# Optimization experiments

Hardware: AMD Instinct MI355X
Metric: run time of the kernel (lower is better)

Reference implementation:

```python
import jax, jax.numpy as jnp
import numpy as np

N = 100000   # nodes per layer
E = 600000   # edges per block
FIN = 256    # raw feature dim
H = 128      # hidden_size
C = 47       # n_classes
L = 3        # num_layers = n_layers + 1
NOUT = 10000 # seed nodes
GEN_EPS = 1e-7
T = 1.0
LN_EPS = 1e-5


def setup_inputs() -> dict:
    key = jax.random.key(0)
    ks = jax.random.split(key, 10)
    return {
        "x": jax.random.normal(ks[0], (N, FIN), jnp.float32),
        "src": jax.random.randint(ks[1], (L - 1, E), 0, N),
        "dst": jax.random.randint(ks[2], (L - 1, E), 0, N),
        "node_map": jax.random.randint(ks[3], (L - 1, N), 0, N),
        "final_map": jax.random.randint(ks[4], (NOUT,), 0, N),
        "enc_w": jax.random.normal(ks[5], (FIN, H), jnp.float32) * 0.05,
        "enc_b": jnp.zeros((H,), jnp.float32),
        "gcn_w": jax.random.normal(ks[6], (L, H, H), jnp.float32) * 0.05,
        "gcn_b": jnp.zeros((L, H), jnp.float32),
        "ln_g": jnp.ones((L, H), jnp.float32),
        "ln_b": jnp.zeros((L, H), jnp.float32),
        "pred_w": jax.random.normal(ks[7], (H, C), jnp.float32) * 0.05,
        "pred_b": jnp.zeros((C,), jnp.float32),
    }


def _layer_norm(h, g, b):
    mu = jnp.mean(h, axis=-1, keepdims=True)
    var = jnp.mean(jnp.square(h - mu), axis=-1, keepdims=True)
    return (h - mu) * jax.lax.rsqrt(var + LN_EPS) * g + b


def _gen_conv(h, src, dst, w, b):
    # GENConv, aggr='softmax', mlp_layers=1, no edge_attr, no msg_norm.
    m = jax.nn.relu(h[src]) + GEN_EPS                      # [E, H] messages
    # per-destination, per-feature segment softmax with temperature T
    mx = jax.ops.segment_max(m * T, dst, num_segments=N)   # [N, H]
    e = jnp.exp(m * T - mx[dst])                           # [E, H]
    denom = jax.ops.segment_sum(e, dst, num_segments=N)    # [N, H]
    alpha = e / (denom[dst] + 1e-16)
    agg = jax.ops.segment_sum(m * alpha, dst, num_segments=N)  # [N, H]
    return (agg + h) @ w + b                               # residual + Linear (MLP)


def reference(x, src, dst, node_map, final_map, enc_w, enc_b,
              gcn_w, gcn_b, ln_g, ln_b, pred_w, pred_b):
    h = x @ enc_w + enc_b                                  # node_features_encoder
    h = _gen_conv(h, src[0], dst[0], gcn_w[0], gcn_b[0])   # gcns[0] with block-0 edges
    for layer in range(1, L):                              # res+ block
        h2 = jax.nn.relu(_layer_norm(h, ln_g[layer - 1], ln_b[layer - 1]))
        # dropout is identity in eval mode (p applied with training=False)
        # gcns[layer] uses the edge_index set BEFORE this iteration's move
        h = _gen_conv(h2, src[layer - 1], dst[layer - 1],
                      gcn_w[layer], gcn_b[layer]) + h
        h = h[node_map[layer - 1]]                         # nf_move_layer_to gather
    h = jax.nn.relu(_layer_norm(h, ln_g[L - 1], ln_b[L - 1]))
    h = h @ pred_w + pred_b                                # node_pred_linear
    h = h[final_map]                                       # seed-node extraction
    return jax.nn.log_softmax(h, axis=-1)
```

## Files before the change

kernel.cpp:

```cpp
#include <hip/hip_runtime.h>
#include <hip/hip_bf16.h>
#include <hip/hip_fp16.h>

typedef unsigned short u16;
typedef unsigned int u32;

#define N_NODES 100000
#define N_EDGES 600000
#define FIN_D   256
#define HDIM    128
#define NCLS    47
#define NOUT_D  10000
#define NCHUNK  196
#define NP2     100352
#define PCH     2048
#define PNB     ((N_EDGES + PCH - 1) / PCH)
#define EB      1024

typedef short bf16x8 __attribute__((ext_vector_type(8)));
typedef float f32x4  __attribute__((ext_vector_type(4)));

#define GPTR(p) (const __attribute__((address_space(1))) u32*)(p)
#define LPTR(p) (__attribute__((address_space(3))) u32*)(p)

__device__ __forceinline__ float bf2f(u16 u) {
    union { u32 i; float f; } v; v.i = ((u32)u) << 16; return v.f;
}
__device__ __forceinline__ u16 f2bf(float f) {
    __hip_bfloat16 h = __float2bfloat16(f);
    return *reinterpret_cast<u16*>(&h);
}
__device__ __forceinline__ float loadF(const void* p, size_t i, bool f32) {
    if (f32) return ((const float*)p)[i];
    return bf2f(((const u16*)p)[i]);
}
__device__ __forceinline__ float wave_sum(float v) {
    #pragma unroll
    for (int o = 32; o > 0; o >>= 1) v += __shfl_xor(v, o, 64);
    return v;
}
__device__ __forceinline__ float wave_max(float v) {
    #pragma unroll
    for (int o = 32; o > 0; o >>= 1) v = fmaxf(v, __shfl_xor(v, o, 64));
    return v;
}
__device__ __forceinline__ int block_excl_scan_256(int v, int* wsum) {
    int lane = threadIdx.x & 63, wv = threadIdx.x >> 6;
    int inc = v;
    #pragma unroll
    for (int off = 1; off < 64; off <<= 1) {
        int u = __shfl_up(inc, off, 64);
        if (lane >= off) inc += u;
    }
    if (lane == 63) wsum[wv] = inc;
    __syncthreads();
    if (threadIdx.x == 0) {
        int a = 0;
        #pragma unroll
        for (int w = 0; w < 4; ++w) { int t = wsum[w]; wsum[w] = a; a += t; }
    }
    __syncthreads();
    return inc - v + wsum[wv];
}

__global__ __launch_bounds__(256) void dtype_detect_kernel(
    const u16* __restrict__ x, int* __restrict__ flag)
{
    int i = blockIdx.x * 256 + threadIdx.x;
    u32 e = (x[i] >> 7) & 0xFF;
    unsigned long long b = __ballot(e >= 200);
    if ((threadIdx.x & 63) == 0) {
        int c = __popcll(b);
        if (c) atomicAdd(&flag[1], c);
    }
}

__global__ __launch_bounds__(256) void histb_kernel(
    const int* __restrict__ dst, int* __restrict__ bcnt, int ebgrid)
{
    __shared__ int h[NCHUNK];
    int half = (blockIdx.x >= ebgrid) ? 1 : 0;
    int e0 = (blockIdx.x - half * ebgrid) * EB;
    for (int i = threadIdx.x; i < NCHUNK; i += 256) h[i] = 0;
    __syncthreads();
    #pragma unroll
    for (int t = 0; t < 4; ++t) {
        int e = e0 + t * 256 + threadIdx.x;
        if (e < N_EDGES) atomicAdd(&h[dst[half * N_EDGES + e] >> 9], 1);
    }
    __syncthreads();
    for (int i = threadIdx.x; i < NCHUNK; i += 256)
        if (h[i]) atomicAdd(&bcnt[half * NCHUNK + i], h[i]);
}

__global__ __launch_bounds__(256) void coff2_kernel(
    const int* __restrict__ csum, int* __restrict__ coff,
    int* __restrict__ bcur)
{
    __shared__ int wsum[4];
    int t = threadIdx.x;
    for (int h = 0; h < 2; ++h) {
        int v = (t < NCHUNK) ? csum[h * NCHUNK + t] : 0;
        int excl = block_excl_scan_256(v, wsum);
        if (t < NCHUNK) {
            coff[h * NCHUNK + t] = excl;
            bcur[(h * NCHUNK + t) * 16] = excl;
        }
        __syncthreads();
    }
}

__global__ __launch_bounds__(256) void bucket_part_kernel(
    const int* __restrict__ src, const int* __restrict__ dst,
    const int* __restrict__ comp1,
    int* __restrict__ bcur, int2* __restrict__ tmp)
{
    __shared__ int hist[NCHUNK];
    __shared__ int base[NCHUNK];
    int half = (blockIdx.x >= PNB) ? 1 : 0;
    int b = blockIdx.x - half * PNB;
    int e0 = b * PCH;
    for (int i = threadIdx.x; i < NCHUNK; i += 256) hist[i] = 0;
    __syncthreads();

    int2 loc[8];
    #pragma unroll
    for (int t = 0; t < 8; ++t) {
        int e = e0 + t * 256 + threadIdx.x;
        loc[t].y = -1;
        if (e < N_EDGES) {
            int ge = half * N_EDGES + e;
            int d = dst[ge];
            int s = src[ge];
            if (half) s = comp1[s];
            loc[t] = make_int2(s, d);
            atomicAdd(&hist[d >> 9], 1);
        }
    }
    __syncthreads();
    for (int i = threadIdx.x; i < NCHUNK; i += 256) {
        int h = hist[i];
        base[i] = (h > 0) ? atomicAdd(&bcur[(half * NCHUNK + i) * 16], h) : 0;
        hist[i] = 0;
    }
    __syncthreads();
    #pragma unroll
    for (int t = 0; t < 8; ++t) {
        if (loc[t].y >= 0) {
            int bk = loc[t].y >> 9;
            int pos = base[bk] + atomicAdd(&hist[bk], 1);
            tmp[(size_t)half * N_EDGES + pos] = loc[t];
        }
    }
}

__global__ __launch_bounds__(256) void bucket_sort_kernel(
    const int2* __restrict__ tmp,
    const int* __restrict__ coff, const int* __restrict__ csum,
    int* __restrict__ rp0, int* __restrict__ rp1,
    int* __restrict__ ei0, int* __restrict__ ei1)
{
    __shared__ int cur[512];
    __shared__ int wsum[4];
    int half = (blockIdx.x >= NCHUNK) ? 1 : 0;
    int b = blockIdx.x - half * NCHUNK;
    int* rp = half ? rp1 : rp0;
    int* ei = half ? ei1 : ei0;
    int n0 = b * 512;
    int beg = coff[half * NCHUNK + b];
    int end = beg + csum[half * NCHUNK + b];
    const int t = threadIdx.x;

    cur[t] = 0; cur[t + 256] = 0;
    __syncthreads();
    for (int i = beg + t; i < end; i += 256)
        atomicAdd(&cur[tmp[(size_t)half * N_EDGES + i].y & 511], 1);
    __syncthreads();

    int d0 = cur[2 * t], d1 = cur[2 * t + 1];
    int excl = block_excl_scan_256(d0 + d1, wsum);
    int base = beg + excl;
    cur[2 * t] = base;
    cur[2 * t + 1] = base + d0;
    if (n0 + 2 * t <= N_NODES)     rp[n0 + 2 * t] = base;
    if (n0 + 2 * t + 1 <= N_NODES) rp[n0 + 2 * t + 1] = base + d0;
    __syncthreads();

    for (int i = beg + t; i < end; i += 256) {
        int2 p = tmp[(size_t)half * N_EDGES + i];
        int pos = atomicAdd(&cur[p.y & 511], 1);
        ei[pos] = p.x;
    }
}

__global__ __launch_bounds__(256) void pack_b_kernel(
    const void* __restrict__ enc_w, const void* __restrict__ gcn_w,
    const int* __restrict__ dt, u16* __restrict__ Bp)
{
    const bool f32 = (dt[1] > 16);
    int o = blockIdx.x * 256 + threadIdx.x;
    if (o >= 32768 + 3 * 16384) return;
    const void* srcp; size_t soff; int m;
    if (o < 32768) { srcp = enc_w; soff = 0; m = o; }
    else {
        int l = (o - 32768) >> 14;
        srcp = gcn_w; soff = (size_t)l * 16384; m = (o - 32768) & 16383;
    }
    int j    = m & 7;
    int lane = (m >> 3) & 63;
    int ct   = (m >> 9) & 7;
    int kidx = m >> 12;
    int k = kidx * 32 + (lane >> 4) * 8 + j;
    int n = ct * 16 + (lane & 15);
    Bp[o] = f2bf(loadF(srcp, soff + (size_t)k * HDIM + n, f32));
}

__global__ __launch_bounds__(256, 2) void enc_gemm_kernel(
    const void* __restrict__ Araw, const u16* __restrict__ Bp,
    const void* __restrict__ bias, const int* __restrict__ dt,
    u16* __restrict__ OutBF)
{
    extern __shared__ char SH[];
    const bool f32 = (dt[1] > 16);
    const int tid  = threadIdx.x;
    const int w    = tid >> 6;
    const int lane = tid & 63;
    const int quad = lane >> 4;
    const int cl   = lane & 15;
    const int m0   = blockIdx.x * 16;

    #pragma unroll
    for (int i = 0; i < 16; ++i) {
        int off = (w * 16 + i) * 1024;
        __builtin_amdgcn_global_load_lds(
            GPTR((const char*)Bp + off + lane * 16),
            LPTR(SH + off), 16, 0, 0);
    }
    if (f32) {
        #pragma unroll
        for (int i = 0; i < 4; ++i) {
            int row = w * 4 + i;
            int src = (lane * 16) ^ ((row & 7) << 4);
            __builtin_amdgcn_global_load_lds(
                GPTR((const char*)Araw + (size_t)(m0 + row) * 1024 + src),
                LPTR(SH + 65536 + row * 1024), 16, 0, 0);
        }
    } else {
        #pragma unroll
        for (int i = 0; i < 2; ++i) {
            int r0 = (w * 2 + i) * 2;
            int row = r0 + (lane >> 5);
            int src = ((lane & 31) * 16) ^ ((row & 7) << 4);
            __builtin_amdgcn_global_load_lds(
                GPTR((const char*)Araw + (size_t)(m0 + row) * 512 + src),
                LPTR(SH + 65536 + r0 * 512), 16, 0, 0);
        }
    }

    f32x4 acc[2];
    acc[0] = (f32x4){0.f, 0.f, 0.f, 0.f};
    acc[1] = (f32x4){0.f, 0.f, 0.f, 0.f};
    const int ct0 = w * 2;
    const int swz = (cl & 7) << 4;

    __syncthreads();

    #pragma unroll
    for (int k = 0; k < 8; ++k) {
        bf16x8 av;
        if (f32) {
            const char* rb = SH + 65536 + cl * 1024;
            int lo = (k * 128 + quad * 32) ^ swz;
            float4 v0 = *(const float4*)(rb + lo);
            float4 v1 = *(const float4*)(rb + (lo ^ 16));
            union { u32 u[4]; bf16x8 v; } cv;
            cv.u[0] = (u32)f2bf(v0.x) | ((u32)f2bf(v0.y) << 16);
            cv.u[1] = (u32)f2bf(v0.z) | ((u32)f2bf(v0.w) << 16);
            cv.u[2] = (u32)f2bf(v1.x) | ((u32)f2bf(v1.y) << 16);
            cv.u[3] = (u32)f2bf(v1.z) | ((u32)f2bf(v1.w) << 16);
            av = cv.v;
        } else {
            const char* rb = SH + 65536 + cl * 512;
            av = *(const bf16x8*)(rb + ((k * 64 + quad * 16) ^ swz));
        }
        #pragma unroll
        for (int c = 0; c < 2; ++c) {
            bf16x8 b = *(const bf16x8*)(SH + k * 8192 + (ct0 + c) * 1024 + lane * 16);
            acc[c] = __builtin_amdgcn_mfma_f32_16x16x32_bf16(av, b, acc[c], 0, 0, 0);
        }
    }

    #pragma unroll
    for (int reg = 0; reg < 4; ++reg) {
        int grow = m0 + quad * 4 + reg;
        #pragma unroll
        for (int c = 0; c < 2; ++c) {
            int col = (ct0 + c) * 16 + cl;
            float v = acc[c][reg] + loadF(bias, col, f32);
            OutBF[(size_t)grow * HDIM + col] = f2bf(v);
        }
    }
}

template<bool OWN_MAP>
__global__ __launch_bounds__(256) void agg_msg_kernel(
    const int* __restrict__ rp, const int* __restrict__ eidx,
    const u16* __restrict__ HBin, const int* __restrict__ own_map,
    u16* __restrict__ Amsg)
{
    __shared__ u32 RS[4][16][64];
    int wave = threadIdx.x >> 6;
    int lane = threadIdx.x & 63;
    int n = blockIdx.x * 4 + wave;
    if (n >= N_NODES) return;
    const u32* HB32 = (const u32*)HBin;
    int nn = OWN_MAP ? own_map[n] : n;
    u32 own = HB32[(size_t)nn * 64 + lane];
    int beg = rp[n], end = rp[n + 1];
    float den0 = 0.f, den1 = 0.f, num0 = 0.f, num1 = 0.f;
    for (int c = beg; c < end; c += 16) {
        int cnt = end - c; if (cnt > 16) cnt = 16;
        int e = c + (lane & 15); if (e > end - 1) e = end - 1;
        int ei = eidx[e];
        int nI = (cnt + 3) >> 2;
        #pragma unroll
        for (int i = 0; i < 4; ++i) {
            if (i < nI) {
                int s = __shfl(ei, i * 4 + (lane >> 4), 64);
                __builtin_amdgcn_global_load_lds(
                    GPTR((const char*)HBin + (size_t)s * 256 + (lane & 15) * 16),
                    LPTR(&RS[wave][i * 4][0]), 16, 0, 0);
            }
        }
        asm volatile("s_waitcnt vmcnt(0)" ::: "memory");
        __builtin_amdgcn_sched_barrier(0);
        #pragma unroll
        for (int t = 0; t < 16; ++t) {
            if (t >= cnt) break;
            u32 h = RS[wave][t][lane];
            float m0 = fmaxf(bf2f((u16)(h & 0xffff)), 0.f) + 1e-7f;
            float m1 = fmaxf(bf2f((u16)(h >> 16)),    0.f) + 1e-7f;
            float e0 = __expf(m0), e1 = __expf(m1);
            den0 += e0; num0 += m0 * e0;
            den1 += e1; num1 += m1 * e1;
        }
        asm volatile("s_waitcnt lgkmcnt(0)" ::: "memory");
        __builtin_amdgcn_sched_barrier(0);
    }
    float a0 = num0 / (den0 + 1e-16f) + bf2f((u16)(own & 0xffff));
    float a1 = num1 / (den1 + 1e-16f) + bf2f((u16)(own >> 16));
    ((u32*)Amsg)[(size_t)n * 64 + lane] = (u32)f2bf(a0) | ((u32)f2bf(a1) << 16);
}

template<bool RES, bool OWN_MAP, bool WRITE_LN>
__global__ __launch_bounds__(256) void conv_gemm_kernel(
    const u16* __restrict__ Amsg, const int* __restrict__ own_map,
    const u16* __restrict__ Bp, int Bpbase,
    const void* __restrict__ bias, int biasoff,
    const __half* __restrict__ Resid,
    const void* __restrict__ lng, const void* __restrict__ lnb, int lnoff,
    const int* __restrict__ dt,
    __half* __restrict__ OutH, u16* __restrict__ HBout)
{
    const bool f32 = (dt[1] > 16);
    __shared__ u16 Bsh[16384];
    __shared__ u16 Ash[8192];
    const int tid  = threadIdx.x;
    const int w    = tid >> 6;
    const int lane = tid & 63;
    const int quad = lane >> 4;
    const int cl   = lane & 15;
    const int m0   = blockIdx.x * 64;

    {
        const char* Bp2 = (const char*)(Bp + Bpbase);
        #pragma unroll
        for (int i = 0; i < 8; ++i)
            __builtin_amdgcn_global_load_lds(
                GPTR(Bp2 + i * 4096 + w * 1024 + lane * 16),
                LPTR((char*)Bsh + i * 4096 + w * 1024), 16, 0, 0);
        const char* Ab = (const char*)Amsg + (size_t)m0 * 256;
        #pragma unroll
        for (int i = 0; i < 4; ++i) {
            int row_local = i * 16 + w * 4 + (lane >> 4);
            int off = ((lane & 15) * 16) ^ ((row_local & 7) << 4);
            __builtin_amdgcn_global_load_lds(
                GPTR(Ab + (size_t)row_local * 256 + off),
                LPTR((char*)Ash + i * 4096 + w * 1024), 16, 0, 0);
        }
    }

    __syncthreads();

    const int row_local = w * 16 + cl;
    const char* ar = (const char*)Ash + row_local * 256;
    const int akey = (row_local & 7) << 4;
    bf16x8 afr[4];
    #pragma unroll
    for (int kidx = 0; kidx < 4; ++kidx)
        afr[kidx] = *(const bf16x8*)(ar + ((kidx * 64 + quad * 16) ^ akey));

    f32x4 acc[8];
    #pragma unroll
    for (int ct = 0; ct < 8; ++ct) acc[ct] = (f32x4){0.f, 0.f, 0.f, 0.f};
    #pragma unroll
    for (int kidx = 0; kidx < 4; ++kidx) {
        const u16* bb = Bsh + ((size_t)(kidx * 8) * 64 + lane) * 8;
        #pragma unroll
        for (int ct = 0; ct < 8; ++ct) {
            bf16x8 b = *(const bf16x8*)(bb + (size_t)ct * 512);
            acc[ct] = __builtin_amdgcn_mfma_f32_16x16x32_bf16(afr[kidx], b, acc[ct], 0, 0, 0);
        }
    }

    #pragma unroll
    for (int reg = 0; reg < 4; ++reg) {
        int n = m0 + w * 16 + quad * 4 + reg;
        if (n >= N_NODES) continue;
        size_t rrow = 0;
        if (RES) rrow = (size_t)(OWN_MAP ? own_map[n] : n) * HDIM;
        float v[8];
        float s1 = 0.f, s2 = 0.f;
        #pragma unroll
        for (int ct = 0; ct < 8; ++ct) {
            int col = ct * 16 + cl;
            float x = acc[ct][reg] + loadF(bias, biasoff + col, f32);
            if (RES) x += __half2float(Resid[rrow + col]);
            v[ct] = x;
            OutH[(size_t)n * HDIM + col] = __float2half(x);
            s1 += x; s2 += x * x;
        }
        if (WRITE_LN) {
            #pragma unroll
            for (int o = 1; o < 16; o <<= 1) {
                s1 += __shfl_xor(s1, o, 64);
                s2 += __shfl_xor(s2, o, 64);
            }
            float mu = s1 * (1.0f / 128.0f);
            float var = s2 * (1.0f / 128.0f) - mu * mu;
            float rs = rsqrtf(fmaxf(var, 0.f) + 1e-5f);
            #pragma unroll
            for (int ct = 0; ct < 8; ++ct) {
                int col = ct * 16 + cl;
                float y = fmaxf((v[ct] - mu) * rs * loadF(lng, lnoff + col, f32)
                                + loadF(lnb, lnoff + col, f32), 0.f);
                HBout[(size_t)n * HDIM + col] = f2bf(y);
            }
        }
    }
}

__global__ __launch_bounds__(256) void final_head_kernel(
    const __half* __restrict__ Hsrc, const int* __restrict__ map1,
    const int* __restrict__ fmap,
    const void* __restrict__ g, const void* __restrict__ b, int goff,
    const void* __restrict__ pw, const void* __restrict__ pb,
    const int* __restrict__ dt, void* __restrict__ out)
{
    const bool f32 = (dt[1] > 16);
    __shared__ float pwl[HDIM * 48];
    __shared__ float pbl[64];
    __shared__ float sh[4][HDIM];
    const int tid = threadIdx.x, wave = tid >> 6, lane = tid & 63;

    for (int i = tid; i < HDIM * NCLS; i += 256)
        pwl[(i / NCLS) * 48 + (i % NCLS)] = loadF(pw, i, f32);
    if (tid < NCLS) pbl[tid] = loadF(pb, tid, f32);
    __syncthreads();

    int i = blockIdx.x * 4 + wave;
    int jj = map1[fmap[i]];
    __half2 hv = *((const __half2*)(Hsrc + (size_t)jj * HDIM) + lane);
    float2 v = __half22float2(hv);
    float mu = wave_sum(v.x + v.y) * (1.0f / 128.0f);
    float d0 = v.x - mu, d1 = v.y - mu;
    float var = wave_sum(d0 * d0 + d1 * d1) * (1.0f / 128.0f);
    float rs = rsqrtf(var + 1e-5f);
    int f0 = lane * 2;
    sh[wave][f0]     = fmaxf(d0 * rs * loadF(g, goff + f0, f32)     + loadF(b, goff + f0, f32),     0.0f);
    sh[wave][f0 + 1] = fmaxf(d1 * rs * loadF(g, goff + f0 + 1, f32) + loadF(b, goff + f0 + 1, f32), 0.0f);
    float acc = -1e30f;
    if (lane < NCLS) {
        acc = pbl[lane];
        #pragma unroll 8
        for (int k = 0; k < HDIM; ++k)
            acc = fmaf(sh[wave][k], pwl[k * 48 + lane], acc);
    }
    float mx = wave_max(acc);
    float ex = (lane < NCLS) ? __expf(acc - mx) : 0.0f;
    float sum = wave_sum(ex);
    if (lane < NCLS) {
        float r = acc - mx - logf(sum);
        if (f32) ((float*)out)[(size_t)i * NCLS + lane] = r;
        else     ((u16*)out)[(size_t)i * NCLS + lane] = f2bf(r);
    }
}

extern "C" void kernel_launch(void* const* d_in, const int* in_sizes, int n_in,
                              void* d_out, int out_size, void* d_ws, size_t ws_size,
                              hipStream_t stream) {
    const void* x       = d_in[0];
    const int* src      = (const int*)d_in[1];
    const int* dst      = (const int*)d_in[2];
    const int* node_map = (const int*)d_in[3];
    const int* fmap     = (const int*)d_in[4];
    const void* enc_w   = d_in[5];
    const void* enc_b   = d_in[6];
    const void* gcn_w   = d_in[7];
    const void* gcn_b   = d_in[8];
    const void* ln_g    = d_in[9];
    const void* ln_b    = d_in[10];
    const void* pred_w  = d_in[11];
    const void* pred_b  = d_in[12];

    char* ws = (char*)d_ws;
    const size_t szH = (size_t)N_NODES * HDIM * sizeof(u16);
    __half* Pa  = (__half*)ws;  ws += szH;
    __half* Pb  = (__half*)ws;  ws += szH;
    u16*   HBa  = (u16*)ws;     ws += szH;
    u16*   HBb  = (u16*)ws;     ws += szH;
    u16*   Amsg = (u16*)ws;     ws += szH;
    int*   FLAG = (int*)ws;     ws += 1024;
    u16*   Bp   = (u16*)ws;     ws += (size_t)(32768 + 3 * 16384) * 2 + 1024;
    int*  rp0   = (int*)ws;  ws += (size_t)(N_NODES + 2) * 4;
    int*  rp1   = (int*)ws;  ws += (size_t)(N_NODES + 2) * 4;
    int*  ei0   = (int*)ws;  ws += (size_t)N_EDGES * 4;
    int*  ei1   = (int*)ws;  ws += (size_t)N_EDGES * 4;
    int2* tmp   = (int2*)ws; ws += (size_t)2 * N_EDGES * 8;
    int*  csum  = (int*)ws;  ws += 2048;
    int*  coff  = (int*)ws;  ws += 2048;
    int*  bcur  = (int*)ws;  ws += (size_t)2 * NCHUNK * 16 * 4 + 1024;

    dim3 blk(256);
    const int ggrid = (N_NODES + 63) / 64;
    const int g16   = (N_NODES + 15) / 16;
    const int ebgrid = (N_EDGES + EB - 1) / EB;
    const int agrid = (N_NODES + 3) / 4;
    const int pgrid = (32768 + 3 * 16384 + 255) / 256;

    hipMemsetAsync(FLAG, 0, 64, stream);
    hipMemsetAsync(csum, 0, 2048, stream);
    dtype_detect_kernel<<<256, blk, 0, stream>>>((const u16*)x, FLAG);
    pack_b_kernel<<<pgrid, blk, 0, stream>>>(enc_w, gcn_w, FLAG, Bp);

    histb_kernel<<<2 * ebgrid, blk, 0, stream>>>(dst, csum, ebgrid);
    coff2_kernel<<<1, blk, 0, stream>>>(csum, coff, bcur);
    bucket_part_kernel<<<2 * PNB, blk, 0, stream>>>(src, dst, node_map, bcur, tmp);
    bucket_sort_kernel<<<2 * NCHUNK, blk, 0, stream>>>(tmp, coff, csum,
                                                       rp0, rp1, ei0, ei1);

    enc_gemm_kernel<<<g16, blk, 81920, stream>>>(x, Bp, enc_b, FLAG, HBa);

    agg_msg_kernel<false><<<agrid, blk, 0, stream>>>(rp0, ei0, HBa, nullptr, Amsg);
    conv_gemm_kernel<false, false, true><<<ggrid, blk, 0, stream>>>(
        Amsg, nullptr, Bp, 32768, gcn_b, 0, nullptr,
        ln_g, ln_b, 0, FLAG, Pa, HBb);

    agg_msg_kernel<false><<<agrid, blk, 0, stream>>>(rp0, ei0, HBb, nullptr, Amsg);
    conv_gemm_kernel<true, false, true><<<ggrid, blk, 0, stream>>>(
        Amsg, nullptr, Bp, 32768 + 16384, gcn_b, 128, Pa,
        ln_g, ln_b, 128, FLAG, Pb, HBa);

    agg_msg_kernel<true><<<agrid, blk, 0, stream>>>(rp1, ei1, HBa, node_map, Amsg);
    conv_gemm_kernel<true, true, false><<<ggrid, blk, 0, stream>>>(
        Amsg, node_map, Bp, 32768 + 2 * 16384, gcn_b, 256, Pb,
        ln_g, ln_b, 256, FLAG, Pa, nullptr);

    final_head_kernel<<<NOUT_D / 4, blk, 0, stream>>>(
        Pa, node_map + N_NODES, fmap, ln_g, ln_b, 256, pred_w, pred_b, FLAG,
        (void*)d_out);
}
```

Before: 543.5 us.

## Pack bucket-sort entries, widen conv GEMM tiles, batch head rows

The bucket-partition temp array now packs each edge as a single u32 (src<<9 | dst&511) instead of an int2, halving that scratch traffic. The conv GEMM processes 128 rows per block (two 16-row MMA tiles per wave), so the B weight tile staged in LDS is reused across twice as many rows, and it gets a launch-bounds occupancy hint. The final head kernel handles 16 seeds per block, which amortises the per-block load of pred weights into shared memory. The costs are more registers and LDS per block, and the packing assumes source indices fit in 23 bits.

```diff
diff --git a/kernel.cpp b/kernel.cpp
--- a/kernel.cpp
+++ b/kernel.cpp
@@ -113,7 +113,7 @@
 __global__ __launch_bounds__(256) void bucket_part_kernel(
     const int* __restrict__ src, const int* __restrict__ dst,
     const int* __restrict__ comp1,
-    int* __restrict__ bcur, int2* __restrict__ tmp)
+    int* __restrict__ bcur, u32* __restrict__ tmp)
 {
     __shared__ int hist[NCHUNK];
     __shared__ int base[NCHUNK];
@@ -149,13 +149,14 @@
         if (loc[t].y >= 0) {
             int bk = loc[t].y >> 9;
             int pos = base[bk] + atomicAdd(&hist[bk], 1);
-            tmp[(size_t)half * N_EDGES + pos] = loc[t];
+            tmp[(size_t)half * N_EDGES + pos] =
+                ((u32)loc[t].x << 9) | ((u32)loc[t].y & 511);
         }
     }
 }
 
 __global__ __launch_bounds__(256) void bucket_sort_kernel(
-    const int2* __restrict__ tmp,
+    const u32* __restrict__ tmp,
     const int* __restrict__ coff, const int* __restrict__ csum,
     int* __restrict__ rp0, int* __restrict__ rp1,
     int* __restrict__ ei0, int* __restrict__ ei1)
@@ -174,7 +175,7 @@
     cur[t] = 0; cur[t + 256] = 0;
     __syncthreads();
     for (int i = beg + t; i < end; i += 256)
-        atomicAdd(&cur[tmp[(size_t)half * N_EDGES + i].y & 511], 1);
+        atomicAdd(&cur[tmp[(size_t)half * N_EDGES + i] & 511], 1);
     __syncthreads();
 
     int d0 = cur[2 * t], d1 = cur[2 * t + 1];
@@ -187,9 +188,9 @@
     __syncthreads();
 
     for (int i = beg + t; i < end; i += 256) {
-        int2 p = tmp[(size_t)half * N_EDGES + i];
-        int pos = atomicAdd(&cur[p.y & 511], 1);
-        ei[pos] = p.x;
+        u32 p = tmp[(size_t)half * N_EDGES + i];
+        int pos = atomicAdd(&cur[p & 511], 1);
+        ei[pos] = (int)(p >> 9);
     }
 }
 
@@ -353,7 +354,7 @@
 }
 
 template<bool RES, bool OWN_MAP, bool WRITE_LN>
-__global__ __launch_bounds__(256) void conv_gemm_kernel(
+__global__ __launch_bounds__(256, 2) void conv_gemm_kernel(
     const u16* __restrict__ Amsg, const int* __restrict__ own_map,
     const u16* __restrict__ Bp, int Bpbase,
     const void* __restrict__ bias, int biasoff,
@@ -364,13 +365,13 @@
 {
     const bool f32 = (dt[1] > 16);
     __shared__ u16 Bsh[16384];
-    __shared__ u16 Ash[8192];
+    __shared__ u16 Ash[16384];
     const int tid  = threadIdx.x;
     const int w    = tid >> 6;
     const int lane = tid & 63;
     const int quad = lane >> 4;
     const int cl   = lane & 15;
-    const int m0   = blockIdx.x * 64;
+    const int m0   = blockIdx.x * 128;
 
     {
         const char* Bp2 = (const char*)(Bp + Bpbase);
@@ -381,7 +382,7 @@
                 LPTR((char*)Bsh + i * 4096 + w * 1024), 16, 0, 0);
         const char* Ab = (const char*)Amsg + (size_t)m0 * 256;
         #pragma unroll
-        for (int i = 0; i < 4; ++i) {
+        for (int i = 0; i < 8; ++i) {
             int row_local = i * 16 + w * 4 + (lane >> 4);
             int off = ((lane & 15) * 16) ^ ((row_local & 7) << 4);
             __builtin_amdgcn_global_load_lds(
@@ -392,59 +393,68 @@
 
     __syncthreads();
 
-    const int row_local = w * 16 + cl;
-    const char* ar = (const char*)Ash + row_local * 256;
-    const int akey = (row_local & 7) << 4;
-    bf16x8 afr[4];
-    #pragma unroll
-    for (int kidx = 0; kidx < 4; ++kidx)
-        afr[kidx] = *(const bf16x8*)(ar + ((kidx * 64 + quad * 16) ^ akey));
-
-    f32x4 acc[8];
-    #pragma unroll
-    for (int ct = 0; ct < 8; ++ct) acc[ct] = (f32x4){0.f, 0.f, 0.f, 0.f};
+    bf16x8 afr[2][4];
+    #pragma unroll
+    for (int t = 0; t < 2; ++t) {
+        const int row_local = w * 32 + t * 16 + cl;
+        const char* ar = (const char*)Ash + row_local * 256;
+        const int akey = (row_local & 7) << 4;
+        #pragma unroll
+        for (int kidx = 0; kidx < 4; ++kidx)
+            afr[t][kidx] = *(const bf16x8*)(ar + ((kidx * 64 + quad * 16) ^ akey));
+    }
+
+    f32x4 acc[2][8];
+    #pragma unroll
+    for (int t = 0; t < 2; ++t)
+        #pragma unroll
+        for (int ct = 0; ct < 8; ++ct) acc[t][ct] = (f32x4){0.f, 0.f, 0.f, 0.f};
     #pragma unroll
     for (int kidx = 0; kidx < 4; ++kidx) {
         const u16* bb = Bsh + ((size_t)(kidx * 8) * 64 + lane) * 8;
         #pragma unroll
         for (int ct = 0; ct < 8; ++ct) {
             bf16x8 b = *(const bf16x8*)(bb + (size_t)ct * 512);
-            acc[ct] = __builtin_amdgcn_mfma_f32_16x16x32_bf16(afr[kidx], b, acc[ct], 0, 0, 0);
-        }
-    }
-
-    #pragma unroll
-    for (int reg = 0; reg < 4; ++reg) {
-        int n = m0 + w * 16 + quad * 4 + reg;
-        if (n >= N_NODES) continue;
-        size_t rrow = 0;
-        if (RES) rrow = (size_t)(OWN_MAP ? own_map[n] : n) * HDIM;
-        float v[8];
-        float s1 = 0.f, s2 = 0.f;
-        #pragma unroll
-        for (int ct = 0; ct < 8; ++ct) {
-            int col = ct * 16 + cl;
-            float x = acc[ct][reg] + loadF(bias, biasoff + col, f32);
-            if (RES) x += __half2float(Resid[rrow + col]);
-            v[ct] = x;
-            OutH[(size_t)n * HDIM + col] = __float2half(x);
-            s1 += x; s2 += x * x;
-        }
-        if (WRITE_LN) {
-            #pragma unroll
-            for (int o = 1; o < 16; o <<= 1) {
-                s1 += __shfl_xor(s1, o, 64);
-                s2 += __shfl_xor(s2, o, 64);
-            }
-            float mu = s1 * (1.0f / 128.0f);
-            float var = s2 * (1.0f / 128.0f) - mu * mu;
-            float rs = rsqrtf(fmaxf(var, 0.f) + 1e-5f);
+            acc[0][ct] = __builtin_amdgcn_mfma_f32_16x16x32_bf16(afr[0][kidx], b, acc[0][ct], 0, 0, 0);
+            acc[1][ct] = __builtin_amdgcn_mfma_f32_16x16x32_bf16(afr[1][kidx], b, acc[1][ct], 0, 0, 0);
+        }
+    }
+
+    #pragma unroll
+    for (int t = 0; t < 2; ++t) {
+        #pragma unroll
+        for (int reg = 0; reg < 4; ++reg) {
+            int n = m0 + w * 32 + t * 16 + quad * 4 + reg;
+            if (n >= N_NODES) continue;
+            size_t rrow = 0;
+            if (RES) rrow = (size_t)(OWN_MAP ? own_map[n] : n) * HDIM;
+            float v[8];
+            float s1 = 0.f, s2 = 0.f;
             #pragma unroll
             for (int ct = 0; ct < 8; ++ct) {
                 int col = ct * 16 + cl;
-                float y = fmaxf((v[ct] - mu) * rs * loadF(lng, lnoff + col, f32)
-                                + loadF(lnb, lnoff + col, f32), 0.f);
-                HBout[(size_t)n * HDIM + col] = f2bf(y);
+                float x = acc[t][ct][reg] + loadF(bias, biasoff + col, f32);
+                if (RES) x += __half2float(Resid[rrow + col]);
+                v[ct] = x;
+                OutH[(size_t)n * HDIM + col] = __float2half(x);
+                s1 += x; s2 += x * x;
+            }
+            if (WRITE_LN) {
+                #pragma unroll
+                for (int o = 1; o < 16; o <<= 1) {
+                    s1 += __shfl_xor(s1, o, 64);
+                    s2 += __shfl_xor(s2, o, 64);
+                }
+                float mu = s1 * (1.0f / 128.0f);
+                float var = s2 * (1.0f / 128.0f) - mu * mu;
+                float rs = rsqrtf(fmaxf(var, 0.f) + 1e-5f);
+                #pragma unroll
+                for (int ct = 0; ct < 8; ++ct) {
+                    int col = ct * 16 + cl;
+                    float y = fmaxf((v[ct] - mu) * rs * loadF(lng, lnoff + col, f32)
+                                    + loadF(lnb, lnoff + col, f32), 0.f);
+                    HBout[(size_t)n * HDIM + col] = f2bf(y);
+                }
             }
         }
     }
@@ -460,7 +470,7 @@
     const bool f32 = (dt[1] > 16);
     __shared__ float pwl[HDIM * 48];
     __shared__ float pbl[64];
-    __shared__ float sh[4][HDIM];
+    __shared__ float sh[4][4][HDIM];
     const int tid = threadIdx.x, wave = tid >> 6, lane = tid & 63;
 
     for (int i = tid; i < HDIM * NCLS; i += 256)
@@ -468,31 +478,34 @@
     if (tid < NCLS) pbl[tid] = loadF(pb, tid, f32);
     __syncthreads();
 
-    int i = blockIdx.x * 4 + wave;
-    int jj = map1[fmap[i]];
-    __half2 hv = *((const __half2*)(Hsrc + (size_t)jj * HDIM) + lane);
-    float2 v = __half22float2(hv);
-    float mu = wave_sum(v.x + v.y) * (1.0f / 128.0f);
-    float d0 = v.x - mu, d1 = v.y - mu;
-    float var = wave_sum(d0 * d0 + d1 * d1) * (1.0f / 128.0f);
-    float rs = rsqrtf(var + 1e-5f);
-    int f0 = lane * 2;
-    sh[wave][f0]     = fmaxf(d0 * rs * loadF(g, goff + f0, f32)     + loadF(b, goff + f0, f32),     0.0f);
-    sh[wave][f0 + 1] = fmaxf(d1 * rs * loadF(g, goff + f0 + 1, f32) + loadF(b, goff + f0 + 1, f32), 0.0f);
-    float acc = -1e30f;
-    if (lane < NCLS) {
-        acc = pbl[lane];
-        #pragma unroll 8
-        for (int k = 0; k < HDIM; ++k)
-            acc = fmaf(sh[wave][k], pwl[k * 48 + lane], acc);
-    }
-    float mx = wave_max(acc);
-    float ex = (lane < NCLS) ? __expf(acc - mx) : 0.0f;
-    float sum = wave_sum(ex);
-    if (lane < NCLS) {
-        float r = acc - mx - logf(sum);
-        if (f32) ((float*)out)[(size_t)i * NCLS + lane] = r;
-        else     ((u16*)out)[(size_t)i * NCLS + lane] = f2bf(r);
+    #pragma unroll
+    for (int js = 0; js < 4; ++js) {
+        int i = blockIdx.x * 16 + wave * 4 + js;
+        int jj = map1[fmap[i]];
+        __half2 hv = *((const __half2*)(Hsrc + (size_t)jj * HDIM) + lane);
+        float2 v = __half22float2(hv);
+        float mu = wave_sum(v.x + v.y) * (1.0f / 128.0f);
+        float d0 = v.x - mu, d1 = v.y - mu;
+        float var = wave_sum(d0 * d0 + d1 * d1) * (1.0f / 128.0f);
+        float rs = rsqrtf(var + 1e-5f);
+        int f0 = lane * 2;
+        sh[wave][js][f0]     = fmaxf(d0 * rs * loadF(g, goff + f0, f32)     + loadF(b, goff + f0, f32),     0.0f);
+        sh[wave][js][f0 + 1] = fmaxf(d1 * rs * loadF(g, goff + f0 + 1, f32) + loadF(b, goff + f0 + 1, f32), 0.0f);
+        float acc = -1e30f;
+        if (lane < NCLS) {
+            acc = pbl[lane];
+            #pragma unroll 8
+            for (int k = 0; k < HDIM; ++k)
+                acc = fmaf(sh[wave][js][k], pwl[k * 48 + lane], acc);
+        }
+        float mx = wave_max(acc);
+        float ex = (lane < NCLS) ? __expf(acc - mx) : 0.0f;
+        float sum = wave_sum(ex);
+        if (lane < NCLS) {
+            float r = acc - mx - logf(sum);
+            if (f32) ((float*)out)[(size_t)i * NCLS + lane] = r;
+            else     ((u16*)out)[(size_t)i * NCLS + lane] = f2bf(r);
+        }
     }
 }
 
@@ -526,13 +539,13 @@
     int*  rp1   = (int*)ws;  ws += (size_t)(N_NODES + 2) * 4;
     int*  ei0   = (int*)ws;  ws += (size_t)N_EDGES * 4;
     int*  ei1   = (int*)ws;  ws += (size_t)N_EDGES * 4;
-    int2* tmp   = (int2*)ws; ws += (size_t)2 * N_EDGES * 8;
+    u32*  tmp   = (u32*)ws;  ws += (size_t)2 * N_EDGES * 4;
     int*  csum  = (int*)ws;  ws += 2048;
     int*  coff  = (int*)ws;  ws += 2048;
     int*  bcur  = (int*)ws;  ws += (size_t)2 * NCHUNK * 16 * 4 + 1024;
 
     dim3 blk(256);
-    const int ggrid = (N_NODES + 63) / 64;
+    const int g128  = (N_NODES + 127) / 128;
     const int g16   = (N_NODES + 15) / 16;
     const int ebgrid = (N_EDGES + EB - 1) / EB;
     const int agrid = (N_NODES + 3) / 4;
@@ -552,21 +565,21 @@
     enc_gemm_kernel<<<g16, blk, 81920, stream>>>(x, Bp, enc_b, FLAG, HBa);
 
     agg_msg_kernel<false><<<agrid, blk, 0, stream>>>(rp0, ei0, HBa, nullptr, Amsg);
-    conv_gemm_kernel<false, false, true><<<ggrid, blk, 0, stream>>>(
+    conv_gemm_kernel<false, false, true><<<g128, blk, 0, stream>>>(
         Amsg, nullptr, Bp, 32768, gcn_b, 0, nullptr,
         ln_g, ln_b, 0, FLAG, Pa, HBb);
 
     agg_msg_kernel<false><<<agrid, blk, 0, stream>>>(rp0, ei0, HBb, nullptr, Amsg);
-    conv_gemm_kernel<true, false, true><<<ggrid, blk, 0, stream>>>(
+    conv_gemm_kernel<true, false, true><<<g128, blk, 0, stream>>>(
         Amsg, nullptr, Bp, 32768 + 16384, gcn_b, 128, Pa,
         ln_g, ln_b, 128, FLAG, Pb, HBa);
 
     agg_msg_kernel<true><<<agrid, blk, 0, stream>>>(rp1, ei1, HBa, node_map, Amsg);
-    conv_gemm_kernel<true, true, false><<<ggrid, blk, 0, stream>>>(
+    conv_gemm_kernel<true, true, false><<<g128, blk, 0, stream>>>(
         Amsg, node_map, Bp, 32768 + 2 * 16384, gcn_b, 256, Pb,
         ln_g, ln_b, 256, FLAG, Pa, nullptr);
 
-    final_head_kernel<<<NOUT_D / 4, blk, 0, stream>>>(
+    final_head_kernel<<<NOUT_D / 16, blk, 0, stream>>>(
         Pa, node_map + N_NODES, fmap, ln_g, ln_b, 256, pred_w, pred_b, FLAG,
         (void*)d_out);
 }
```

New measurement: 581.8 us. +7.1%, slower.
